# Performance work log

Measured on AMD Instinct MI355X. Metric: run time of the kernel, lower is better.

The kernel has to match this reference:

```python
import jax, jax.numpy as jnp
import numpy as np

N_PER_G, G = 2048, 2
N = N_PER_G * G
CIN, COUT, WIDTH, K = 128, 256, 64, 16
R_BASE, BOX, SLOPE = 1.8, 16.0, 0.1
R1, L1, O1 = 1.5 * R_BASE, 5, WIDTH // 2
R2, L2, O2 = R_BASE, 7, WIDTH // 4
R3, L3, O3 = 0.75 * R_BASE, 11, WIDTH // 4


def _build_edges(pos, batch, r):
    srcs, dsts = [], []
    for g in range(G):
        idx = np.nonzero(batch == g)[0]
        p = pos[idx]
        d2 = ((p[:, None, :] - p[None, :, :]) ** 2).sum(-1)
        i, j = np.nonzero(d2 <= r * r)  # includes self-pairs, like torch_cluster.radius
        dsts.append(idx[i]); srcs.append(idx[j])
    return (np.concatenate(srcs).astype(np.int32), np.concatenate(dsts).astype(np.int32))


def setup_inputs() -> dict:
    rng = np.random.default_rng(0)
    pos = (rng.random((N, 3)) * BOX).astype(np.float32)
    batch = np.repeat(np.arange(G), N_PER_G).astype(np.int32)
    seq = np.tile(np.arange(N_PER_G), G).astype(np.int32)
    ori = np.linalg.qr(rng.standard_normal((N, 3, 3)))[0].reshape(N, 9).astype(np.float32)
    x = rng.standard_normal((N, CIN)).astype(np.float32)
    s1, d1 = _build_edges(pos, batch, R1)
    s2, d2 = _build_edges(pos, batch, R2)
    s3, d3 = _build_edges(pos, batch, R3)
    def p(*shape):
        return jnp.asarray((rng.standard_normal(shape) * 0.05).astype(np.float32))
    return dict(
        x=jnp.asarray(x), pos=jnp.asarray(pos), ori=jnp.asarray(ori),
        seq=jnp.asarray(seq), batch=jnp.asarray(batch),
        src1=jnp.asarray(s1), dst1=jnp.asarray(d1),
        src2=jnp.asarray(s2), dst2=jnp.asarray(d2),
        src3=jnp.asarray(s3), dst3=jnp.asarray(d3),
        id_bn_g=jnp.ones(CIN), id_bn_b=jnp.zeros(CIN), id_W=p(CIN, COUT),
        in_bn_g=jnp.ones(CIN), in_bn_b=jnp.zeros(CIN), in_W=p(CIN, WIDTH),
        mid_bn_g=jnp.ones(WIDTH), mid_bn_b=jnp.zeros(WIDTH),
        Ws1=p(L1, 7, K), bs1=p(L1, K), W1=p(K * WIDTH, O1),
        Ws2=p(L2, 7, K), bs2=p(L2, K), W2=p(K * WIDTH, O2),
        Ws3=p(L3, 7, K), bs3=p(L3, K), W3=p(K * WIDTH, O3),
        out_bn_g=jnp.ones(WIDTH), out_bn_b=jnp.zeros(WIDTH), out_W=p(WIDTH, COUT),
    )


def _bn(x, g, b):
    # BatchNorm1d forward with batch statistics (biased variance), eps=1e-5
    m = jnp.mean(x, axis=0)
    v = jnp.mean((x - m) ** 2, axis=0)
    return (x - m) * jax.lax.rsqrt(v + 1e-5) * g + b


def _cdconv(h, pos, seq, ori, src, dst, r, l, Ws, bs, W):
    # src = sender j, dst = receiver i
    delta = pos[src] - pos[dst]                               # [E,3]
    dist = jnp.linalg.norm(delta, axis=-1, keepdims=True)     # [E,1]
    dirn = delta / (dist + 1e-9)
    fr_i = ori[dst].reshape(-1, 3, 3)
    fr_j = ori[src].reshape(-1, 3, 3)
    pos_feat = jnp.einsum('eij,ej->ei', fr_i, dirn)           # direction in receiver's local frame
    ori_feat = jnp.sum(fr_i * fr_j, axis=-1)                  # frame-axis dot products [E,3]
    feat = jnp.concatenate([dist / r, pos_feat, ori_feat], axis=-1)  # [E,7]
    hl = l // 2
    idx = jnp.clip(seq[src] - seq[dst], -hl, hl) + hl         # discrete sequential bin in [0,l-1]
    w = jax.nn.leaky_relu(jnp.einsum('ec,eck->ek', feat, Ws[idx]) + bs[idx], 0.2)  # [E,K]
    msg = (w[:, :, None] * h[src][:, None, :]).reshape(w.shape[0], -1)  # [E, K*C]
    agg = jax.ops.segment_sum(msg, dst, num_segments=h.shape[0])        # [N, K*C]
    return agg @ W


def _forward(x, pos, ori, seq, src1, dst1, src2, dst2, src3, dst3,
             id_bn_g, id_bn_b, id_W, in_bn_g, in_bn_b, in_W, mid_bn_g, mid_bn_b,
             Ws1, bs1, W1, Ws2, bs2, W2, Ws3, bs3, W3, out_bn_g, out_bn_b, out_W):
    identity = jax.nn.leaky_relu(_bn(x, id_bn_g, id_bn_b), SLOPE) @ id_W
    h = jax.nn.leaky_relu(_bn(x, in_bn_g, in_bn_b), SLOPE) @ in_W
    h = jax.nn.leaky_relu(_bn(h, mid_bn_g, mid_bn_b), SLOPE)
    x1 = _cdconv(h, pos, seq, ori, src1, dst1, R1, L1, Ws1, bs1, W1)
    x2 = _cdconv(h, pos, seq, ori, src2, dst2, R2, L2, Ws2, bs2, W2)
    x3 = _cdconv(h, pos, seq, ori, src3, dst3, R3, L3, Ws3, bs3, W3)
    cat = jnp.concatenate([x1, x2, x3], axis=1)               # [N, WIDTH]
    return jax.nn.leaky_relu(_bn(cat, out_bn_g, out_bn_b), SLOPE) @ out_W + identity


def reference(x, pos, ori, seq, batch, src1, dst1, src2, dst2, src3, dst3,
              id_bn_g, id_bn_b, id_W, in_bn_g, in_bn_b, in_W, mid_bn_g, mid_bn_b,
              Ws1, bs1, W1, Ws2, bs2, W2, Ws3, bs3, W3, out_bn_g, out_bn_b, out_W):
    return _forward(x, pos, ori, seq, src1, dst1, src2, dst2, src3, dst3,
                    id_bn_g, id_bn_b, id_W, in_bn_g, in_bn_b, in_W, mid_bn_g, mid_bn_b,
                    Ws1, bs1, W1, Ws2, bs2, W2, Ws3, bs3, W3, out_bn_g, out_bn_b, out_W)
```

## Files before the change

kernel.cpp:

```cpp
#include <hip/hip_runtime.h>

#define N_NODES 4096
#define CIN     128
#define COUT    256
#define WIDTH   64
#define KDIM    16
#define SLOPE   0.1f
#define WSLOPE  0.2f
#define BN_EPS  1e-5f

typedef float float4u __attribute__((ext_vector_type(4), aligned(4)));

__device__ __forceinline__ float lrelu(float x, float s) { return x > 0.f ? x : s * x; }

struct EdgeP {
  const int* src; const int* dst;
  const float* Ws; const float* bs;
  float* wbuf; int E; float inv_r; int hl;
};

#define WS_LD 113
#define BS_LD 17
#define NB_STATSX 32
#define NB_ROWPTR 49

__global__ __launch_bounds__(256) void prep_kernel(
    const float* __restrict__ x,
    const float* __restrict__ id_g, const float* __restrict__ id_b,
    const float* __restrict__ in_g, const float* __restrict__ in_b,
    float* __restrict__ sA, float* __restrict__ hA,
    float* __restrict__ sB, float* __restrict__ hB,
    int* __restrict__ rowp,
    EdgeP e0, EdgeP e1, EdgeP e2,
    const float* __restrict__ pos, const float* __restrict__ ori,
    const int* __restrict__ seq,
    int nb1, int nb2)
{
  int bx = blockIdx.x, t = threadIdx.x;

  if (bx < NB_STATSX) {
    int cg = bx;
    int lane = t & 63, wv = t >> 6;
    float s[4] = {0.f, 0.f, 0.f, 0.f}, q[4] = {0.f, 0.f, 0.f, 0.f};
    for (int r = t; r < N_NODES; r += 256) {
      float4u a = *(const float4u*)(x + (size_t)r * CIN + cg * 4);
      float v[4] = {a.x, a.y, a.z, a.w};
#pragma unroll
      for (int i = 0; i < 4; i++) { s[i] += v[i]; q[i] += v[i] * v[i]; }
    }
#pragma unroll
    for (int m = 1; m < 64; m <<= 1) {
#pragma unroll
      for (int i = 0; i < 4; i++) { s[i] += __shfl_xor(s[i], m, 64); q[i] += __shfl_xor(q[i], m, 64); }
    }
    __shared__ float rs[4][4], rq[4][4];
    if (lane == 0) {
#pragma unroll
      for (int i = 0; i < 4; i++) { rs[wv][i] = s[i]; rq[wv][i] = q[i]; }
    }
    __syncthreads();
    if (t < 4) {
      float S = rs[0][t] + rs[1][t] + rs[2][t] + rs[3][t];
      float Q = rq[0][t] + rq[1][t] + rq[2][t] + rq[3][t];
      float m = S / N_NODES;
      float v = Q / N_NODES - m * m;
      float rsv = rsqrtf(v + BN_EPS);
      int c = cg * 4 + t;
      float sa = id_g[c] * rsv;
      float sb = in_g[c] * rsv;
      sA[c] = sa; hA[c] = id_b[c] - m * sa;
      sB[c] = sb; hB[c] = in_b[c] - m * sb;
    }
    return;
  }

  if (bx < NB_STATSX + NB_ROWPTR) {
    int idx = (bx - NB_STATSX) * 256 + t;
    if (idx >= 3 * (N_NODES + 1)) return;
    int b = idx / (N_NODES + 1);
    int n = idx % (N_NODES + 1);
    const int* d = (b == 0) ? e0.dst : (b == 1) ? e1.dst : e2.dst;
    int E = (b == 0) ? e0.E : (b == 1) ? e1.E : e2.E;
    int lo = 0, hi = E;
    if (n >= N_NODES) lo = E;
    else {
      while (lo < hi) { int mid = (lo + hi) >> 1; if (d[mid] < n) lo = mid + 1; else hi = mid; }
    }
    rowp[(size_t)b * (N_NODES + 1) + n] = lo;
    return;
  }

  int eb = bx - (NB_STATSX + NB_ROWPTR);
  EdgeP p;
  int base;
  if (eb < nb1)            { p = e0; base = eb; }
  else if (eb < nb1 + nb2) { p = e1; base = eb - nb1; }
  else                     { p = e2; base = eb - nb1 - nb2; }

  __shared__ float wsl[11 * WS_LD];
  __shared__ float bsl[11 * BS_LD];
  int L = 2 * p.hl + 1;
  for (int i = t; i < L * 112; i += 256) {
    int bin = i / 112, r = i - bin * 112;
    wsl[bin * WS_LD + r] = p.Ws[(size_t)bin * 112 + r];
  }
  for (int i = t; i < L * 16; i += 256) {
    int bin = i >> 4, r = i & 15;
    bsl[bin * BS_LD + r] = p.bs[(size_t)bin * 16 + r];
  }
  __syncthreads();

  int e = base * 256 + t;
  if (e >= p.E) return;
  int j = p.src[e], i = p.dst[e];
  float px = pos[j * 3 + 0] - pos[i * 3 + 0];
  float py = pos[j * 3 + 1] - pos[i * 3 + 1];
  float pz = pos[j * 3 + 2] - pos[i * 3 + 2];
  float fi[9], fj[9];
  {
    float4u a0 = *(const float4u*)(ori + (size_t)i * 9);
    float4u a1 = *(const float4u*)(ori + (size_t)i * 9 + 4);
    fi[0] = a0.x; fi[1] = a0.y; fi[2] = a0.z; fi[3] = a0.w;
    fi[4] = a1.x; fi[5] = a1.y; fi[6] = a1.z; fi[7] = a1.w;
    fi[8] = ori[(size_t)i * 9 + 8];
    float4u b0 = *(const float4u*)(ori + (size_t)j * 9);
    float4u b1 = *(const float4u*)(ori + (size_t)j * 9 + 4);
    fj[0] = b0.x; fj[1] = b0.y; fj[2] = b0.z; fj[3] = b0.w;
    fj[4] = b1.x; fj[5] = b1.y; fj[6] = b1.z; fj[7] = b1.w;
    fj[8] = ori[(size_t)j * 9 + 8];
  }
  float dist = sqrtf(px * px + py * py + pz * pz);
  float inv = 1.0f / (dist + 1e-9f);
  float dx = px * inv, dy = py * inv, dz = pz * inv;
  float feat[7];
  feat[0] = dist * p.inv_r;
  feat[1] = fi[0] * dx + fi[1] * dy + fi[2] * dz;
  feat[2] = fi[3] * dx + fi[4] * dy + fi[5] * dz;
  feat[3] = fi[6] * dx + fi[7] * dy + fi[8] * dz;
  feat[4] = fi[0] * fj[0] + fi[1] * fj[1] + fi[2] * fj[2];
  feat[5] = fi[3] * fj[3] + fi[4] * fj[4] + fi[5] * fj[5];
  feat[6] = fi[6] * fj[6] + fi[7] * fj[7] + fi[8] * fj[8];
  int d = seq[j] - seq[i];
  d = d < -p.hl ? -p.hl : (d > p.hl ? p.hl : d);
  int bin = d + p.hl;
  const float* Wp = wsl + bin * WS_LD;
  const float* bp = bsl + bin * BS_LD;
  float w16[KDIM];
#pragma unroll
  for (int k = 0; k < KDIM; k++) {
    float a = bp[k];
#pragma unroll
    for (int c = 0; c < 7; c++) a += feat[c] * Wp[c * KDIM + k];
    w16[k] = lrelu(a, WSLOPE);
  }
  float4* wb = (float4*)(p.wbuf + (size_t)e * KDIM);
#pragma unroll
  for (int k = 0; k < 4; k++)
    wb[k] = make_float4(w16[4 * k], w16[4 * k + 1], w16[4 * k + 2], w16[4 * k + 3]);
}

__global__ __launch_bounds__(256) void gemm2_kernel(
    const float* __restrict__ x,
    const float* __restrict__ sA, const float* __restrict__ hA,
    const float* __restrict__ sB, const float* __restrict__ hB,
    const float* __restrict__ idW, const float* __restrict__ inW,
    float* __restrict__ ident, float* __restrict__ hpre)
{
  int bx = blockIdx.x, t = threadIdx.x;
  __shared__ float at[8 * CIN];
  bool coutp = bx < 512;
  int n0 = (coutp ? bx : bx - 512) * 8;
  {
    int r = t >> 5, c4 = (t & 31) * 4;
    const float* S = coutp ? sA : sB;
    const float* H = coutp ? hA : hB;
    float4u xv = *(const float4u*)(x + (size_t)(n0 + r) * CIN + c4);
    float4u sv = *(const float4u*)(S + c4);
    float4u hv = *(const float4u*)(H + c4);
    float4u o;
    o.x = lrelu(xv.x * sv.x + hv.x, SLOPE);
    o.y = lrelu(xv.y * sv.y + hv.y, SLOPE);
    o.z = lrelu(xv.z * sv.z + hv.z, SLOPE);
    o.w = lrelu(xv.w * sv.w + hv.w, SLOPE);
    *(float4u*)(at + r * CIN + c4) = o;
  }
  __syncthreads();
  if (coutp) {
    float acc[8] = {0.f, 0.f, 0.f, 0.f, 0.f, 0.f, 0.f, 0.f};
    for (int k = 0; k < CIN; k += 4) {
      float w0 = idW[(size_t)(k + 0) * COUT + t];
      float w1 = idW[(size_t)(k + 1) * COUT + t];
      float w2 = idW[(size_t)(k + 2) * COUT + t];
      float w3 = idW[(size_t)(k + 3) * COUT + t];
#pragma unroll
      for (int r8 = 0; r8 < 8; r8++) {
        float4u a = *(const float4u*)(at + r8 * CIN + k);
        acc[r8] += a.x * w0 + a.y * w1 + a.z * w2 + a.w * w3;
      }
    }
#pragma unroll
    for (int r8 = 0; r8 < 8; r8++) ident[(size_t)(n0 + r8) * COUT + t] = acc[r8];
  } else {
    int j = t & 63, g = t >> 6;
    float a0 = 0.f, a1 = 0.f;
    for (int k = 0; k < CIN; k += 4) {
      float w0 = inW[(size_t)(k + 0) * WIDTH + j];
      float w1 = inW[(size_t)(k + 1) * WIDTH + j];
      float w2 = inW[(size_t)(k + 2) * WIDTH + j];
      float w3 = inW[(size_t)(k + 3) * WIDTH + j];
      float4u u = *(const float4u*)(at + (2 * g) * CIN + k);
      float4u v = *(const float4u*)(at + (2 * g + 1) * CIN + k);
      a0 += u.x * w0 + u.y * w1 + u.z * w2 + u.w * w3;
      a1 += v.x * w0 + v.y * w1 + v.z * w2 + v.w * w3;
    }
    hpre[(size_t)(n0 + 2 * g) * WIDTH + j] = a0;
    hpre[(size_t)(n0 + 2 * g + 1) * WIDTH + j] = a1;
  }
}

__global__ __launch_bounds__(256) void stats_affine_kernel(
    const float* __restrict__ X, int C,
    const float* __restrict__ g, const float* __restrict__ b,
    float* __restrict__ s_out, float* __restrict__ h_out)
{
  int cg = blockIdx.x;
  int t = threadIdx.x, lane = t & 63, wv = t >> 6;
  float s[4] = {0.f, 0.f, 0.f, 0.f}, q[4] = {0.f, 0.f, 0.f, 0.f};
  for (int r = t; r < N_NODES; r += 256) {
    float4u a = *(const float4u*)(X + (size_t)r * C + cg * 4);
    float v[4] = {a.x, a.y, a.z, a.w};
#pragma unroll
    for (int i = 0; i < 4; i++) { s[i] += v[i]; q[i] += v[i] * v[i]; }
  }
#pragma unroll
  for (int m = 1; m < 64; m <<= 1) {
#pragma unroll
    for (int i = 0; i < 4; i++) { s[i] += __shfl_xor(s[i], m, 64); q[i] += __shfl_xor(q[i], m, 64); }
  }
  __shared__ float rs[4][4], rq[4][4];
  if (lane == 0) {
#pragma unroll
    for (int i = 0; i < 4; i++) { rs[wv][i] = s[i]; rq[wv][i] = q[i]; }
  }
  __syncthreads();
  if (t < 4) {
    float S = rs[0][t] + rs[1][t] + rs[2][t] + rs[3][t];
    float Q = rq[0][t] + rq[1][t] + rq[2][t] + rq[3][t];
    float m = S / N_NODES;
    float v = Q / N_NODES - m * m;
    int c = cg * 4 + t;
    float sv = g[c] * rsqrtf(v + BN_EPS);
    s_out[c] = sv;
    h_out[c] = b[c] - m * sv;
  }
}

struct AggP {
  const int* src; const float* wbuf; const float* Wf;
  int O; int coloff;
};

#define ALD 68

__global__ __launch_bounds__(256) void agg3_kernel(
    AggP p0, AggP p1, AggP p2, const int* __restrict__ rowp,
    const float* __restrict__ hpre,
    const float* __restrict__ sH, const float* __restrict__ hH,
    float* __restrict__ cat)
{
  int b = blockIdx.y;
  AggP p = (b == 0) ? p0 : (b == 1) ? p1 : p2;
  int n = blockIdx.x, t = threadIdx.x, lane = t & 63, wv = t >> 6;

  __shared__ float lds[4][KDIM * ALD];
  __shared__ float pw[4][WIDTH];

  float scH = sH[lane], shH = hH[lane];
  const int* rp = rowp + (size_t)b * (N_NODES + 1);
  int start = rp[n], end = rp[n + 1];

  float acc[KDIM];
#pragma unroll
  for (int k = 0; k < KDIM; k++) acc[k] = 0.f;

  int e = start + wv;
  for (; e + 12 < end; e += 16) {
    int j0 = __builtin_amdgcn_readfirstlane(p.src[e]);
    int j1 = __builtin_amdgcn_readfirstlane(p.src[e + 4]);
    int j2 = __builtin_amdgcn_readfirstlane(p.src[e + 8]);
    int j3 = __builtin_amdgcn_readfirstlane(p.src[e + 12]);
    float r0 = hpre[(size_t)j0 * WIDTH + lane];
    float r1 = hpre[(size_t)j1 * WIDTH + lane];
    float r2 = hpre[(size_t)j2 * WIDTH + lane];
    float r3 = hpre[(size_t)j3 * WIDTH + lane];
    const float4* a0 = (const float4*)(p.wbuf + (size_t)e * KDIM);
    const float4* a1 = (const float4*)(p.wbuf + (size_t)(e + 4) * KDIM);
    const float4* a2 = (const float4*)(p.wbuf + (size_t)(e + 8) * KDIM);
    const float4* a3 = (const float4*)(p.wbuf + (size_t)(e + 12) * KDIM);
    float4 w00 = a0[0], w01 = a0[1], w02 = a0[2], w03 = a0[3];
    float4 w10 = a1[0], w11 = a1[1], w12 = a1[2], w13 = a1[3];
    float4 w20 = a2[0], w21 = a2[1], w22 = a2[2], w23 = a2[3];
    float4 w30 = a3[0], w31 = a3[1], w32 = a3[2], w33 = a3[3];
    float hj0 = lrelu(r0 * scH + shH, SLOPE);
    float hj1 = lrelu(r1 * scH + shH, SLOPE);
    float hj2 = lrelu(r2 * scH + shH, SLOPE);
    float hj3 = lrelu(r3 * scH + shH, SLOPE);
    acc[0] += w00.x * hj0; acc[1] += w00.y * hj0; acc[2] += w00.z * hj0; acc[3] += w00.w * hj0;
    acc[4] += w01.x * hj0; acc[5] += w01.y * hj0; acc[6] += w01.z * hj0; acc[7] += w01.w * hj0;
    acc[8] += w02.x * hj0; acc[9] += w02.y * hj0; acc[10] += w02.z * hj0; acc[11] += w02.w * hj0;
    acc[12] += w03.x * hj0; acc[13] += w03.y * hj0; acc[14] += w03.z * hj0; acc[15] += w03.w * hj0;
    acc[0] += w10.x * hj1; acc[1] += w10.y * hj1; acc[2] += w10.z * hj1; acc[3] += w10.w * hj1;
    acc[4] += w11.x * hj1; acc[5] += w11.y * hj1; acc[6] += w11.z * hj1; acc[7] += w11.w * hj1;
    acc[8] += w12.x * hj1; acc[9] += w12.y * hj1; acc[10] += w12.z * hj1; acc[11] += w12.w * hj1;
    acc[12] += w13.x * hj1; acc[13] += w13.y * hj1; acc[14] += w13.z * hj1; acc[15] += w13.w * hj1;
    acc[0] += w20.x * hj2; acc[1] += w20.y * hj2; acc[2] += w20.z * hj2; acc[3] += w20.w * hj2;
    acc[4] += w21.x * hj2; acc[5] += w21.y * hj2; acc[6] += w21.z * hj2; acc[7] += w21.w * hj2;
    acc[8] += w22.x * hj2; acc[9] += w22.y * hj2; acc[10] += w22.z * hj2; acc[11] += w22.w * hj2;
    acc[12] += w23.x * hj2; acc[13] += w23.y * hj2; acc[14] += w23.z * hj2; acc[15] += w23.w * hj2;
    acc[0] += w30.x * hj3; acc[1] += w30.y * hj3; acc[2] += w30.z * hj3; acc[3] += w30.w * hj3;
    acc[4] += w31.x * hj3; acc[5] += w31.y * hj3; acc[6] += w31.z * hj3; acc[7] += w31.w * hj3;
    acc[8] += w32.x * hj3; acc[9] += w32.y * hj3; acc[10] += w32.z * hj3; acc[11] += w32.w * hj3;
    acc[12] += w33.x * hj3; acc[13] += w33.y * hj3; acc[14] += w33.z * hj3; acc[15] += w33.w * hj3;
  }
  for (; e < end; e += 4) {
    int j = __builtin_amdgcn_readfirstlane(p.src[e]);
    float hr = hpre[(size_t)j * WIDTH + lane];
    const float4* w4 = (const float4*)(p.wbuf + (size_t)e * KDIM);
    float4 w0 = w4[0], w1 = w4[1], w2 = w4[2], w3 = w4[3];
    float hj = lrelu(hr * scH + shH, SLOPE);
    acc[0] += w0.x * hj; acc[1] += w0.y * hj; acc[2] += w0.z * hj; acc[3] += w0.w * hj;
    acc[4] += w1.x * hj; acc[5] += w1.y * hj; acc[6] += w1.z * hj; acc[7] += w1.w * hj;
    acc[8] += w2.x * hj; acc[9] += w2.y * hj; acc[10] += w2.z * hj; acc[11] += w2.w * hj;
    acc[12] += w3.x * hj; acc[13] += w3.y * hj; acc[14] += w3.z * hj; acc[15] += w3.w * hj;
  }

#pragma unroll
  for (int k = 0; k < KDIM; k++) lds[wv][k * ALD + lane] = acc[k];
  __syncthreads();

  for (int i = t; i < KDIM * ALD; i += 256)
    lds[0][i] = lds[0][i] + lds[1][i] + lds[2][i] + lds[3][i];
  __syncthreads();

  int O = p.O;
  int o = t & (O - 1);
  int q = t / O;
  int kpg = O >> 4;
  float part = 0.f;
  for (int kk = 0; kk < kpg; kk++) {
    int k = q * kpg + kk;
    const float* ar = lds[0] + k * ALD;
    const float* wf = p.Wf + (size_t)(k * WIDTH) * O + o;
    for (int c = 0; c < WIDTH; c += 4) {
      float4 a = *(const float4*)(ar + c);
      part += a.x * wf[(size_t)(c + 0) * O];
      part += a.y * wf[(size_t)(c + 1) * O];
      part += a.z * wf[(size_t)(c + 2) * O];
      part += a.w * wf[(size_t)(c + 3) * O];
    }
  }
  for (int m = O; m < 64; m <<= 1) part += __shfl_xor(part, m, 64);
  if (lane < O) pw[wv][lane] = part;
  __syncthreads();
  if (t < O)
    cat[(size_t)n * WIDTH + p.coloff + t] = pw[0][t] + pw[1][t] + pw[2][t] + pw[3][t];
}

__global__ __launch_bounds__(256) void final_kernel(
    const float* __restrict__ cat,
    const float* __restrict__ sC, const float* __restrict__ hC,
    const float* __restrict__ outW,
    const float* __restrict__ identity, float* __restrict__ out)
{
  int t = threadIdx.x;
  int n0 = blockIdx.x * 8;
  __shared__ float cn8[8 * WIDTH];
#pragma unroll
  for (int s = 0; s < 2; s++) {
    int ii = s * 256 + t;
    int r = ii >> 6, k = ii & 63;
    cn8[ii] = lrelu(cat[(size_t)(n0 + r) * WIDTH + k] * sC[k] + hC[k], SLOPE);
  }
  __syncthreads();
  float acc[8];
#pragma unroll
  for (int r = 0; r < 8; r++) acc[r] = identity[(size_t)(n0 + r) * COUT + t];
  for (int k = 0; k < WIDTH; k += 4) {
    float w0 = outW[(size_t)(k + 0) * COUT + t];
    float w1 = outW[(size_t)(k + 1) * COUT + t];
    float w2 = outW[(size_t)(k + 2) * COUT + t];
    float w3 = outW[(size_t)(k + 3) * COUT + t];
#pragma unroll
    for (int r = 0; r < 8; r++) {
      float4u a = *(const float4u*)(cn8 + r * WIDTH + k);
      acc[r] += a.x * w0 + a.y * w1 + a.z * w2 + a.w * w3;
    }
  }
#pragma unroll
  for (int r = 0; r < 8; r++) out[(size_t)(n0 + r) * COUT + t] = acc[r];
}

extern "C" void kernel_launch(void* const* d_in, const int* in_sizes, int n_in,
                              void* d_out, int out_size, void* d_ws, size_t ws_size,
                              hipStream_t stream) {
  const float* x    = (const float*)d_in[0];
  const float* pos  = (const float*)d_in[1];
  const float* ori  = (const float*)d_in[2];
  const int* seq  = (const int*)d_in[3];
  const int* src1 = (const int*)d_in[5];  const int* dst1 = (const int*)d_in[6];
  const int* src2 = (const int*)d_in[7];  const int* dst2 = (const int*)d_in[8];
  const int* src3 = (const int*)d_in[9];  const int* dst3 = (const int*)d_in[10];
  const float* id_g  = (const float*)d_in[11]; const float* id_b  = (const float*)d_in[12];
  const float* id_W  = (const float*)d_in[13];
  const float* in_g  = (const float*)d_in[14]; const float* in_b  = (const float*)d_in[15];
  const float* in_W  = (const float*)d_in[16];
  const float* mid_g = (const float*)d_in[17]; const float* mid_b = (const float*)d_in[18];
  const float* Ws1   = (const float*)d_in[19]; const float* bs1   = (const float*)d_in[20];
  const float* W1    = (const float*)d_in[21];
  const float* Ws2   = (const float*)d_in[22]; const float* bs2   = (const float*)d_in[23];
  const float* W2    = (const float*)d_in[24];
  const float* Ws3   = (const float*)d_in[25]; const float* bs3   = (const float*)d_in[26];
  const float* W3    = (const float*)d_in[27];
  const float* out_g = (const float*)d_in[28]; const float* out_b = (const float*)d_in[29];
  const float* out_W = (const float*)d_in[30];

  const int E1 = in_sizes[5], E2 = in_sizes[7], E3 = in_sizes[9];

  float* wsp = (float*)d_ws;
  size_t off = 0;
  auto alloc = [&](size_t n) { float* p = wsp + off; off += (n + 63) & ~(size_t)63; return p; };
  float* sA   = alloc(CIN);   float* hA = alloc(CIN);
  float* sB   = alloc(CIN);   float* hB = alloc(CIN);
  float* sH   = alloc(WIDTH); float* hH = alloc(WIDTH);
  float* sC   = alloc(WIDTH); float* hC = alloc(WIDTH);
  float* ident = alloc((size_t)N_NODES * COUT);
  float* hpre  = alloc((size_t)N_NODES * WIDTH);
  float* catb  = alloc((size_t)N_NODES * WIDTH);
  int*   rowp  = (int*)alloc(3 * (N_NODES + 1));
  float* w1    = alloc((size_t)E1 * KDIM);
  float* w2    = alloc((size_t)E2 * KDIM);
  float* w3    = alloc((size_t)E3 * KDIM);
  (void)ws_size; (void)n_in; (void)out_size;

  int nb1 = (E1 + 255) / 256, nb2 = (E2 + 255) / 256, nb3 = (E3 + 255) / 256;

  EdgeP e0{src1, dst1, Ws1, bs1, w1, E1, 1.0f / 2.70f, 2};
  EdgeP e1{src2, dst2, Ws2, bs2, w2, E2, 1.0f / 1.80f, 3};
  EdgeP e2{src3, dst3, Ws3, bs3, w3, E3, 1.0f / 1.35f, 5};

  prep_kernel<<<NB_STATSX + NB_ROWPTR + nb1 + nb2 + nb3, 256, 0, stream>>>(
      x, id_g, id_b, in_g, in_b, sA, hA, sB, hB, rowp,
      e0, e1, e2, pos, ori, seq, nb1, nb2);
  gemm2_kernel<<<1024, 256, 0, stream>>>(x, sA, hA, sB, hB, id_W, in_W, ident, hpre);
  stats_affine_kernel<<<WIDTH / 4, 256, 0, stream>>>(hpre, WIDTH, mid_g, mid_b, sH, hH);
  AggP a0{src1, w1, W1, 32, 0};
  AggP a1{src2, w2, W2, 16, 32};
  AggP a2{src3, w3, W3, 16, 48};
  agg3_kernel<<<dim3(N_NODES, 3), 256, 0, stream>>>(a0, a1, a2, rowp, hpre, sH, hH, catb);
  stats_affine_kernel<<<WIDTH / 4, 256, 0, stream>>>(catb, WIDTH, out_g, out_b, sC, hC);
  final_kernel<<<N_NODES / 8, 256, 0, stream>>>(catb, sC, hC, out_W, ident, (float*)d_out);
}
```

Measured before the change: 233.9 us.

## Fuse BN stats into producers via atomics; aggregate four nodes per block

Removes both stats_affine kernel launches. Their column sums and sums of squares are now accumulated with atomicAdd at the end of gemm2 and agg3, and the scale and shift are recomputed locally in the consumer kernels. agg3 now gives each wave its own node (4 nodes per block) instead of splitting one node's edges across four waves, so the cross-wave LDS reduction goes away and each Wf load is reused for four nodes. The cost is atomic contention on 256 floats, non-deterministic summation order, and possible imbalance when nodes have very different degrees.

```diff
diff --git a/kernel.cpp b/kernel.cpp
--- a/kernel.cpp
+++ b/kernel.cpp
@@ -13,6 +13,7 @@
 
 __device__ __forceinline__ float lrelu(float x, float s) { return x > 0.f ? x : s * x; }
 
+
 struct EdgeP {
   const int* src; const int* dst;
   const float* Ws; const float* bs;
@@ -30,7 +31,7 @@
     const float* __restrict__ in_g, const float* __restrict__ in_b,
     float* __restrict__ sA, float* __restrict__ hA,
     float* __restrict__ sB, float* __restrict__ hB,
-    int* __restrict__ rowp,
+    int* __restrict__ rowp, float* __restrict__ accum,
     EdgeP e0, EdgeP e1, EdgeP e2,
     const float* __restrict__ pos, const float* __restrict__ ori,
     const int* __restrict__ seq,
@@ -39,6 +40,7 @@
   int bx = blockIdx.x, t = threadIdx.x;
 
   if (bx < NB_STATSX) {
+    if (bx == 0) accum[t] = 0.f;
     int cg = bx;
     int lane = t & 63, wv = t >> 6;
     float s[4] = {0.f, 0.f, 0.f, 0.f}, q[4] = {0.f, 0.f, 0.f, 0.f};
@@ -164,7 +166,8 @@
     const float* __restrict__ sA, const float* __restrict__ hA,
     const float* __restrict__ sB, const float* __restrict__ hB,
     const float* __restrict__ idW, const float* __restrict__ inW,
-    float* __restrict__ ident, float* __restrict__ hpre)
+    float* __restrict__ ident, float* __restrict__ hpre,
+    float* __restrict__ accum)
 {
   int bx = blockIdx.x, t = threadIdx.x;
   __shared__ float at[8 * CIN];
@@ -215,43 +218,14 @@
     }
     hpre[(size_t)(n0 + 2 * g) * WIDTH + j] = a0;
     hpre[(size_t)(n0 + 2 * g + 1) * WIDTH + j] = a1;
-  }
-}
-
-__global__ __launch_bounds__(256) void stats_affine_kernel(
-    const float* __restrict__ X, int C,
-    const float* __restrict__ g, const float* __restrict__ b,
-    float* __restrict__ s_out, float* __restrict__ h_out)
-{
-  int cg = blockIdx.x;
-  int t = threadIdx.x, lane = t & 63, wv = t >> 6;
-  float s[4] = {0.f, 0.f, 0.f, 0.f}, q[4] = {0.f, 0.f, 0.f, 0.f};
-  for (int r = t; r < N_NODES; r += 256) {
-    float4u a = *(const float4u*)(X + (size_t)r * C + cg * 4);
-    float v[4] = {a.x, a.y, a.z, a.w};
-#pragma unroll
-    for (int i = 0; i < 4; i++) { s[i] += v[i]; q[i] += v[i] * v[i]; }
-  }
-#pragma unroll
-  for (int m = 1; m < 64; m <<= 1) {
-#pragma unroll
-    for (int i = 0; i < 4; i++) { s[i] += __shfl_xor(s[i], m, 64); q[i] += __shfl_xor(q[i], m, 64); }
-  }
-  __shared__ float rs[4][4], rq[4][4];
-  if (lane == 0) {
-#pragma unroll
-    for (int i = 0; i < 4; i++) { rs[wv][i] = s[i]; rq[wv][i] = q[i]; }
-  }
-  __syncthreads();
-  if (t < 4) {
-    float S = rs[0][t] + rs[1][t] + rs[2][t] + rs[3][t];
-    float Q = rq[0][t] + rq[1][t] + rq[2][t] + rq[3][t];
-    float m = S / N_NODES;
-    float v = Q / N_NODES - m * m;
-    int c = cg * 4 + t;
-    float sv = g[c] * rsqrtf(v + BN_EPS);
-    s_out[c] = sv;
-    h_out[c] = b[c] - m * sv;
+    __shared__ float ps[4][WIDTH], pq[4][WIDTH];
+    ps[g][j] = a0 + a1;
+    pq[g][j] = a0 * a0 + a1 * a1;
+    __syncthreads();
+    if (t < WIDTH) {
+      atomicAdd(&accum[t],      ps[0][t] + ps[1][t] + ps[2][t] + ps[3][t]);
+      atomicAdd(&accum[64 + t], pq[0][t] + pq[1][t] + pq[2][t] + pq[3][t]);
+    }
   }
 }
 
@@ -261,46 +235,53 @@
 };
 
 #define ALD 68
+#define STRIP (KDIM * ALD + 4)
 
 __global__ __launch_bounds__(256) void agg3_kernel(
     AggP p0, AggP p1, AggP p2, const int* __restrict__ rowp,
     const float* __restrict__ hpre,
-    const float* __restrict__ sH, const float* __restrict__ hH,
-    float* __restrict__ cat)
+    const float* __restrict__ mid_g, const float* __restrict__ mid_b,
+    float* __restrict__ accum, float* __restrict__ cat)
 {
   int b = blockIdx.y;
   AggP p = (b == 0) ? p0 : (b == 1) ? p1 : p2;
-  int n = blockIdx.x, t = threadIdx.x, lane = t & 63, wv = t >> 6;
-
-  __shared__ float lds[4][KDIM * ALD];
-  __shared__ float pw[4][WIDTH];
-
-  float scH = sH[lane], shH = hH[lane];
+  int n0 = blockIdx.x * 4, t = threadIdx.x, lane = t & 63, wv = t >> 6;
+
+  __shared__ float lds[4 * STRIP];
+  __shared__ float pw[4][4][32];
+  __shared__ float sHl[WIDTH], hHl[WIDTH];
+  if (t < WIDTH) {
+    float m = accum[t] * (1.f / N_NODES);
+    float v = accum[64 + t] * (1.f / N_NODES) - m * m;
+    float s = mid_g[t] * rsqrtf(v + BN_EPS);
+    sHl[t] = s; hHl[t] = mid_b[t] - m * s;
+  }
+  __syncthreads();
+  float scH = sHl[lane], shH = hHl[lane];
+
   const int* rp = rowp + (size_t)b * (N_NODES + 1);
+  int n = n0 + wv;
   int start = rp[n], end = rp[n + 1];
 
   float acc[KDIM];
 #pragma unroll
   for (int k = 0; k < KDIM; k++) acc[k] = 0.f;
 
-  int e = start + wv;
-  for (; e + 12 < end; e += 16) {
+  int e = start;
+  for (; e + 3 < end; e += 4) {
     int j0 = __builtin_amdgcn_readfirstlane(p.src[e]);
-    int j1 = __builtin_amdgcn_readfirstlane(p.src[e + 4]);
-    int j2 = __builtin_amdgcn_readfirstlane(p.src[e + 8]);
-    int j3 = __builtin_amdgcn_readfirstlane(p.src[e + 12]);
+    int j1 = __builtin_amdgcn_readfirstlane(p.src[e + 1]);
+    int j2 = __builtin_amdgcn_readfirstlane(p.src[e + 2]);
+    int j3 = __builtin_amdgcn_readfirstlane(p.src[e + 3]);
     float r0 = hpre[(size_t)j0 * WIDTH + lane];
     float r1 = hpre[(size_t)j1 * WIDTH + lane];
     float r2 = hpre[(size_t)j2 * WIDTH + lane];
     float r3 = hpre[(size_t)j3 * WIDTH + lane];
     const float4* a0 = (const float4*)(p.wbuf + (size_t)e * KDIM);
-    const float4* a1 = (const float4*)(p.wbuf + (size_t)(e + 4) * KDIM);
-    const float4* a2 = (const float4*)(p.wbuf + (size_t)(e + 8) * KDIM);
-    const float4* a3 = (const float4*)(p.wbuf + (size_t)(e + 12) * KDIM);
-    float4 w00 = a0[0], w01 = a0[1], w02 = a0[2], w03 = a0[3];
-    float4 w10 = a1[0], w11 = a1[1], w12 = a1[2], w13 = a1[3];
-    float4 w20 = a2[0], w21 = a2[1], w22 = a2[2], w23 = a2[3];
-    float4 w30 = a3[0], w31 = a3[1], w32 = a3[2], w33 = a3[3];
+    float4 w00 = a0[0], w01 = a0[1], w02 = a0[2],  w03 = a0[3];
+    float4 w10 = a0[4], w11 = a0[5], w12 = a0[6],  w13 = a0[7];
+    float4 w20 = a0[8], w21 = a0[9], w22 = a0[10], w23 = a0[11];
+    float4 w30 = a0[12], w31 = a0[13], w32 = a0[14], w33 = a0[15];
     float hj0 = lrelu(r0 * scH + shH, SLOPE);
     float hj1 = lrelu(r1 * scH + shH, SLOPE);
     float hj2 = lrelu(r2 * scH + shH, SLOPE);
@@ -322,7 +303,7 @@
     acc[8] += w32.x * hj3; acc[9] += w32.y * hj3; acc[10] += w32.z * hj3; acc[11] += w32.w * hj3;
     acc[12] += w33.x * hj3; acc[13] += w33.y * hj3; acc[14] += w33.z * hj3; acc[15] += w33.w * hj3;
   }
-  for (; e < end; e += 4) {
+  for (; e < end; e++) {
     int j = __builtin_amdgcn_readfirstlane(p.src[e]);
     float hr = hpre[(size_t)j * WIDTH + lane];
     const float4* w4 = (const float4*)(p.wbuf + (size_t)e * KDIM);
@@ -335,46 +316,65 @@
   }
 
 #pragma unroll
-  for (int k = 0; k < KDIM; k++) lds[wv][k * ALD + lane] = acc[k];
-  __syncthreads();
-
-  for (int i = t; i < KDIM * ALD; i += 256)
-    lds[0][i] = lds[0][i] + lds[1][i] + lds[2][i] + lds[3][i];
+  for (int k = 0; k < KDIM; k++) lds[wv * STRIP + k * ALD + lane] = acc[k];
   __syncthreads();
 
   int O = p.O;
   int o = t & (O - 1);
   int q = t / O;
   int kpg = O >> 4;
-  float part = 0.f;
+  float part[4] = {0.f, 0.f, 0.f, 0.f};
   for (int kk = 0; kk < kpg; kk++) {
     int k = q * kpg + kk;
-    const float* ar = lds[0] + k * ALD;
     const float* wf = p.Wf + (size_t)(k * WIDTH) * O + o;
     for (int c = 0; c < WIDTH; c += 4) {
-      float4 a = *(const float4*)(ar + c);
-      part += a.x * wf[(size_t)(c + 0) * O];
-      part += a.y * wf[(size_t)(c + 1) * O];
-      part += a.z * wf[(size_t)(c + 2) * O];
-      part += a.w * wf[(size_t)(c + 3) * O];
-    }
-  }
-  for (int m = O; m < 64; m <<= 1) part += __shfl_xor(part, m, 64);
-  if (lane < O) pw[wv][lane] = part;
-  __syncthreads();
-  if (t < O)
-    cat[(size_t)n * WIDTH + p.coloff + t] = pw[0][t] + pw[1][t] + pw[2][t] + pw[3][t];
+      float w0 = wf[(size_t)(c + 0) * O];
+      float w1 = wf[(size_t)(c + 1) * O];
+      float w2 = wf[(size_t)(c + 2) * O];
+      float w3 = wf[(size_t)(c + 3) * O];
+#pragma unroll
+      for (int r = 0; r < 4; r++) {
+        float4 a = *(const float4*)(lds + r * STRIP + k * ALD + c);
+        part[r] += a.x * w0 + a.y * w1 + a.z * w2 + a.w * w3;
+      }
+    }
+  }
+  for (int m = O; m < 64; m <<= 1) {
+#pragma unroll
+    for (int r = 0; r < 4; r++) part[r] += __shfl_xor(part[r], m, 64);
+  }
+  if (lane < O) {
+#pragma unroll
+    for (int r = 0; r < 4; r++) pw[wv][r][lane] = part[r];
+  }
+  __syncthreads();
+  if (t < 4 * O) {
+    int r = t / O, o2 = t % O;
+    float v = pw[0][r][o2] + pw[1][r][o2] + pw[2][r][o2] + pw[3][r][o2];
+    cat[(size_t)(n0 + r) * WIDTH + p.coloff + o2] = v;
+    atomicAdd(&accum[128 + p.coloff + o2], v);
+    atomicAdd(&accum[192 + p.coloff + o2], v * v);
+  }
 }
 
 __global__ __launch_bounds__(256) void final_kernel(
     const float* __restrict__ cat,
-    const float* __restrict__ sC, const float* __restrict__ hC,
+    const float* __restrict__ out_g, const float* __restrict__ out_b,
+    const float* __restrict__ accum,
     const float* __restrict__ outW,
     const float* __restrict__ identity, float* __restrict__ out)
 {
   int t = threadIdx.x;
   int n0 = blockIdx.x * 8;
+  __shared__ float sC[WIDTH], hC[WIDTH];
   __shared__ float cn8[8 * WIDTH];
+  if (t < WIDTH) {
+    float m = accum[128 + t] * (1.f / N_NODES);
+    float v = accum[192 + t] * (1.f / N_NODES) - m * m;
+    float s = out_g[t] * rsqrtf(v + BN_EPS);
+    sC[t] = s; hC[t] = out_b[t] - m * s;
+  }
+  __syncthreads();
 #pragma unroll
   for (int s = 0; s < 2; s++) {
     int ii = s * 256 + t;
@@ -429,10 +429,9 @@
   float* wsp = (float*)d_ws;
   size_t off = 0;
   auto alloc = [&](size_t n) { float* p = wsp + off; off += (n + 63) & ~(size_t)63; return p; };
+  float* accum = alloc(256);
   float* sA   = alloc(CIN);   float* hA = alloc(CIN);
   float* sB   = alloc(CIN);   float* hB = alloc(CIN);
-  float* sH   = alloc(WIDTH); float* hH = alloc(WIDTH);
-  float* sC   = alloc(WIDTH); float* hC = alloc(WIDTH);
   float* ident = alloc((size_t)N_NODES * COUT);
   float* hpre  = alloc((size_t)N_NODES * WIDTH);
   float* catb  = alloc((size_t)N_NODES * WIDTH);
@@ -449,14 +448,14 @@
   EdgeP e2{src3, dst3, Ws3, bs3, w3, E3, 1.0f / 1.35f, 5};
 
   prep_kernel<<<NB_STATSX + NB_ROWPTR + nb1 + nb2 + nb3, 256, 0, stream>>>(
-      x, id_g, id_b, in_g, in_b, sA, hA, sB, hB, rowp,
+      x, id_g, id_b, in_g, in_b, sA, hA, sB, hB, rowp, accum,
       e0, e1, e2, pos, ori, seq, nb1, nb2);
-  gemm2_kernel<<<1024, 256, 0, stream>>>(x, sA, hA, sB, hB, id_W, in_W, ident, hpre);
-  stats_affine_kernel<<<WIDTH / 4, 256, 0, stream>>>(hpre, WIDTH, mid_g, mid_b, sH, hH);
+  gemm2_kernel<<<1024, 256, 0, stream>>>(x, sA, hA, sB, hB, id_W, in_W, ident, hpre, accum);
   AggP a0{src1, w1, W1, 32, 0};
   AggP a1{src2, w2, W2, 16, 32};
   AggP a2{src3, w3, W3, 16, 48};
-  agg3_kernel<<<dim3(N_NODES, 3), 256, 0, stream>>>(a0, a1, a2, rowp, hpre, sH, hH, catb);
-  stats_affine_kernel<<<WIDTH / 4, 256, 0, stream>>>(catb, WIDTH, out_g, out_b, sC, hC);
-  final_kernel<<<N_NODES / 8, 256, 0, stream>>>(catb, sC, hC, out_W, ident, (float*)d_out);
+  agg3_kernel<<<dim3(N_NODES / 4, 3), 256, 0, stream>>>(a0, a1, a2, rowp, hpre,
+                                                        mid_g, mid_b, accum, catb);
+  final_kernel<<<N_NODES / 8, 256, 0, stream>>>(catb, out_g, out_b, accum, out_W,
+                                                ident, (float*)d_out);
 }
```

Measured after the change: 529.7 us. 126% more time.

## Fuse BatchNorm statistics into producer kernels via striped atomic accumulators

Applied to the files above, without the earlier changes.

Removes the two standalone stats_affine kernels by accumulating per-channel sum and sum-of-squares with atomics into 32 striped buffers inside gemm2 (for hpre) and agg3 (for cat). The buffers are zeroed in prep_kernel. Consumers (agg3, final) reduce the stripes and compute the scale/shift themselves, which saves two launches and two full re-reads of the activations. In exchange it adds atomic traffic and a redundant per-block reduction over 32 stripes in every agg3 and final block, and the float atomics make summation order nondeterministic.

```diff
diff --git a/kernel.cpp b/kernel.cpp
--- a/kernel.cpp
+++ b/kernel.cpp
@@ -8,6 +8,7 @@
 #define SLOPE   0.1f
 #define WSLOPE  0.2f
 #define BN_EPS  1e-5f
+#define NSTRIPE 32
 
 typedef float float4u __attribute__((ext_vector_type(4), aligned(4)));
 
@@ -30,7 +31,7 @@
     const float* __restrict__ in_g, const float* __restrict__ in_b,
     float* __restrict__ sA, float* __restrict__ hA,
     float* __restrict__ sB, float* __restrict__ hB,
-    int* __restrict__ rowp,
+    int* __restrict__ rowp, float* __restrict__ accum,
     EdgeP e0, EdgeP e1, EdgeP e2,
     const float* __restrict__ pos, const float* __restrict__ ori,
     const int* __restrict__ seq,
@@ -39,6 +40,7 @@
   int bx = blockIdx.x, t = threadIdx.x;
 
   if (bx < NB_STATSX) {
+    accum[bx * 256 + t] = 0.f;
     int cg = bx;
     int lane = t & 63, wv = t >> 6;
     float s[4] = {0.f, 0.f, 0.f, 0.f}, q[4] = {0.f, 0.f, 0.f, 0.f};
@@ -164,7 +166,8 @@
     const float* __restrict__ sA, const float* __restrict__ hA,
     const float* __restrict__ sB, const float* __restrict__ hB,
     const float* __restrict__ idW, const float* __restrict__ inW,
-    float* __restrict__ ident, float* __restrict__ hpre)
+    float* __restrict__ ident, float* __restrict__ hpre,
+    float* __restrict__ accum)
 {
   int bx = blockIdx.x, t = threadIdx.x;
   __shared__ float at[8 * CIN];
@@ -215,43 +218,15 @@
     }
     hpre[(size_t)(n0 + 2 * g) * WIDTH + j] = a0;
     hpre[(size_t)(n0 + 2 * g + 1) * WIDTH + j] = a1;
-  }
-}
-
-__global__ __launch_bounds__(256) void stats_affine_kernel(
-    const float* __restrict__ X, int C,
-    const float* __restrict__ g, const float* __restrict__ b,
-    float* __restrict__ s_out, float* __restrict__ h_out)
-{
-  int cg = blockIdx.x;
-  int t = threadIdx.x, lane = t & 63, wv = t >> 6;
-  float s[4] = {0.f, 0.f, 0.f, 0.f}, q[4] = {0.f, 0.f, 0.f, 0.f};
-  for (int r = t; r < N_NODES; r += 256) {
-    float4u a = *(const float4u*)(X + (size_t)r * C + cg * 4);
-    float v[4] = {a.x, a.y, a.z, a.w};
-#pragma unroll
-    for (int i = 0; i < 4; i++) { s[i] += v[i]; q[i] += v[i] * v[i]; }
-  }
-#pragma unroll
-  for (int m = 1; m < 64; m <<= 1) {
-#pragma unroll
-    for (int i = 0; i < 4; i++) { s[i] += __shfl_xor(s[i], m, 64); q[i] += __shfl_xor(q[i], m, 64); }
-  }
-  __shared__ float rs[4][4], rq[4][4];
-  if (lane == 0) {
-#pragma unroll
-    for (int i = 0; i < 4; i++) { rs[wv][i] = s[i]; rq[wv][i] = q[i]; }
-  }
-  __syncthreads();
-  if (t < 4) {
-    float S = rs[0][t] + rs[1][t] + rs[2][t] + rs[3][t];
-    float Q = rq[0][t] + rq[1][t] + rq[2][t] + rq[3][t];
-    float m = S / N_NODES;
-    float v = Q / N_NODES - m * m;
-    int c = cg * 4 + t;
-    float sv = g[c] * rsqrtf(v + BN_EPS);
-    s_out[c] = sv;
-    h_out[c] = b[c] - m * sv;
+    __shared__ float ps[4][WIDTH], pq[4][WIDTH];
+    ps[g][j] = a0 + a1;
+    pq[g][j] = a0 * a0 + a1 * a1;
+    __syncthreads();
+    if (t < WIDTH) {
+      float* as = accum + (bx & (NSTRIPE - 1)) * 256;
+      atomicAdd(&as[t],      ps[0][t] + ps[1][t] + ps[2][t] + ps[3][t]);
+      atomicAdd(&as[64 + t], pq[0][t] + pq[1][t] + pq[2][t] + pq[3][t]);
+    }
   }
 }
 
@@ -265,8 +240,8 @@
 __global__ __launch_bounds__(256) void agg3_kernel(
     AggP p0, AggP p1, AggP p2, const int* __restrict__ rowp,
     const float* __restrict__ hpre,
-    const float* __restrict__ sH, const float* __restrict__ hH,
-    float* __restrict__ cat)
+    const float* __restrict__ mid_g, const float* __restrict__ mid_b,
+    float* __restrict__ accum, float* __restrict__ cat)
 {
   int b = blockIdx.y;
   AggP p = (b == 0) ? p0 : (b == 1) ? p1 : p2;
@@ -274,8 +249,22 @@
 
   __shared__ float lds[4][KDIM * ALD];
   __shared__ float pw[4][WIDTH];
-
-  float scH = sH[lane], shH = hH[lane];
+  __shared__ float sHl[WIDTH], hHl[WIDTH];
+  if (t < WIDTH) {
+    float S = 0.f, Q = 0.f;
+#pragma unroll
+    for (int s = 0; s < NSTRIPE; s++) {
+      S += accum[s * 256 + t];
+      Q += accum[s * 256 + 64 + t];
+    }
+    float m = S * (1.f / N_NODES);
+    float v = Q * (1.f / N_NODES) - m * m;
+    float sc = mid_g[t] * rsqrtf(v + BN_EPS);
+    sHl[t] = sc; hHl[t] = mid_b[t] - m * sc;
+  }
+  __syncthreads();
+  float scH = sHl[lane], shH = hHl[lane];
+
   const int* rp = rowp + (size_t)b * (N_NODES + 1);
   int start = rp[n], end = rp[n + 1];
 
@@ -362,19 +351,39 @@
   for (int m = O; m < 64; m <<= 1) part += __shfl_xor(part, m, 64);
   if (lane < O) pw[wv][lane] = part;
   __syncthreads();
-  if (t < O)
-    cat[(size_t)n * WIDTH + p.coloff + t] = pw[0][t] + pw[1][t] + pw[2][t] + pw[3][t];
+  if (t < O) {
+    float v = pw[0][t] + pw[1][t] + pw[2][t] + pw[3][t];
+    cat[(size_t)n * WIDTH + p.coloff + t] = v;
+    float* as = accum + (n & (NSTRIPE - 1)) * 256;
+    atomicAdd(&as[128 + p.coloff + t], v);
+    atomicAdd(&as[192 + p.coloff + t], v * v);
+  }
 }
 
 __global__ __launch_bounds__(256) void final_kernel(
     const float* __restrict__ cat,
-    const float* __restrict__ sC, const float* __restrict__ hC,
+    const float* __restrict__ out_g, const float* __restrict__ out_b,
+    const float* __restrict__ accum,
     const float* __restrict__ outW,
     const float* __restrict__ identity, float* __restrict__ out)
 {
   int t = threadIdx.x;
   int n0 = blockIdx.x * 8;
+  __shared__ float sC[WIDTH], hC[WIDTH];
   __shared__ float cn8[8 * WIDTH];
+  if (t < WIDTH) {
+    float S = 0.f, Q = 0.f;
+#pragma unroll
+    for (int s = 0; s < NSTRIPE; s++) {
+      S += accum[s * 256 + 128 + t];
+      Q += accum[s * 256 + 192 + t];
+    }
+    float m = S * (1.f / N_NODES);
+    float v = Q * (1.f / N_NODES) - m * m;
+    float sc = out_g[t] * rsqrtf(v + BN_EPS);
+    sC[t] = sc; hC[t] = out_b[t] - m * sc;
+  }
+  __syncthreads();
 #pragma unroll
   for (int s = 0; s < 2; s++) {
     int ii = s * 256 + t;
@@ -429,10 +438,9 @@
   float* wsp = (float*)d_ws;
   size_t off = 0;
   auto alloc = [&](size_t n) { float* p = wsp + off; off += (n + 63) & ~(size_t)63; return p; };
+  float* accum = alloc(NSTRIPE * 256);
   float* sA   = alloc(CIN);   float* hA = alloc(CIN);
   float* sB   = alloc(CIN);   float* hB = alloc(CIN);
-  float* sH   = alloc(WIDTH); float* hH = alloc(WIDTH);
-  float* sC   = alloc(WIDTH); float* hC = alloc(WIDTH);
   float* ident = alloc((size_t)N_NODES * COUT);
   float* hpre  = alloc((size_t)N_NODES * WIDTH);
   float* catb  = alloc((size_t)N_NODES * WIDTH);
@@ -449,14 +457,14 @@
   EdgeP e2{src3, dst3, Ws3, bs3, w3, E3, 1.0f / 1.35f, 5};
 
   prep_kernel<<<NB_STATSX + NB_ROWPTR + nb1 + nb2 + nb3, 256, 0, stream>>>(
-      x, id_g, id_b, in_g, in_b, sA, hA, sB, hB, rowp,
+      x, id_g, id_b, in_g, in_b, sA, hA, sB, hB, rowp, accum,
       e0, e1, e2, pos, ori, seq, nb1, nb2);
-  gemm2_kernel<<<1024, 256, 0, stream>>>(x, sA, hA, sB, hB, id_W, in_W, ident, hpre);
-  stats_affine_kernel<<<WIDTH / 4, 256, 0, stream>>>(hpre, WIDTH, mid_g, mid_b, sH, hH);
+  gemm2_kernel<<<1024, 256, 0, stream>>>(x, sA, hA, sB, hB, id_W, in_W, ident, hpre, accum);
   AggP a0{src1, w1, W1, 32, 0};
   AggP a1{src2, w2, W2, 16, 32};
   AggP a2{src3, w3, W3, 16, 48};
-  agg3_kernel<<<dim3(N_NODES, 3), 256, 0, stream>>>(a0, a1, a2, rowp, hpre, sH, hH, catb);
-  stats_affine_kernel<<<WIDTH / 4, 256, 0, stream>>>(catb, WIDTH, out_g, out_b, sC, hC);
-  final_kernel<<<N_NODES / 8, 256, 0, stream>>>(catb, sC, hC, out_W, ident, (float*)d_out);
+  agg3_kernel<<<dim3(N_NODES, 3), 256, 0, stream>>>(a0, a1, a2, rowp, hpre,
+                                                    mid_g, mid_b, accum, catb);
+  final_kernel<<<N_NODES / 8, 256, 0, stream>>>(catb, out_g, out_b, accum, out_W,
+                                                ident, (float*)d_out);
 }
```

Measured after the change: 233.0 us. About the same (-0.4%).

## Process two nodes per block in agg3 to reuse projection weights

Applied to the files above, without the earlier changes.

The aggregation kernel now handles two destination nodes per block, with two waves per node splitting that node's edges. In the final projection each weight value loaded from global memory is applied to both nodes' aggregated features, halving weight traffic per node and halving the block count. In exchange, each node's edge loop has only two waves instead of four, so per-node latency hiding drops and nodes with different degrees can leave waves unbalanced.

```diff
diff --git a/kernel.cpp b/kernel.cpp
--- a/kernel.cpp
+++ b/kernel.cpp
@@ -270,12 +270,17 @@
 {
   int b = blockIdx.y;
   AggP p = (b == 0) ? p0 : (b == 1) ? p1 : p2;
-  int n = blockIdx.x, t = threadIdx.x, lane = t & 63, wv = t >> 6;
+  int nA = blockIdx.x * 2, t = threadIdx.x, lane = t & 63, wv = t >> 6;
 
   __shared__ float lds[4][KDIM * ALD];
-  __shared__ float pw[4][WIDTH];
-
-  float scH = sH[lane], shH = hH[lane];
+  __shared__ float pw[4][2][32];
+  __shared__ float sHl[WIDTH], hHl[WIDTH];
+  if (t < WIDTH) { sHl[t] = sH[t]; hHl[t] = hH[t]; }
+  __syncthreads();
+  float scH = sHl[lane], shH = hHl[lane];
+
+  int n = nA + (wv >> 1);
+  int sub = wv & 1;
   const int* rp = rowp + (size_t)b * (N_NODES + 1);
   int start = rp[n], end = rp[n + 1];
 
@@ -283,20 +288,20 @@
 #pragma unroll
   for (int k = 0; k < KDIM; k++) acc[k] = 0.f;
 
-  int e = start + wv;
-  for (; e + 12 < end; e += 16) {
+  int e = start + sub;
+  for (; e + 6 < end; e += 8) {
     int j0 = __builtin_amdgcn_readfirstlane(p.src[e]);
-    int j1 = __builtin_amdgcn_readfirstlane(p.src[e + 4]);
-    int j2 = __builtin_amdgcn_readfirstlane(p.src[e + 8]);
-    int j3 = __builtin_amdgcn_readfirstlane(p.src[e + 12]);
+    int j1 = __builtin_amdgcn_readfirstlane(p.src[e + 2]);
+    int j2 = __builtin_amdgcn_readfirstlane(p.src[e + 4]);
+    int j3 = __builtin_amdgcn_readfirstlane(p.src[e + 6]);
     float r0 = hpre[(size_t)j0 * WIDTH + lane];
     float r1 = hpre[(size_t)j1 * WIDTH + lane];
     float r2 = hpre[(size_t)j2 * WIDTH + lane];
     float r3 = hpre[(size_t)j3 * WIDTH + lane];
     const float4* a0 = (const float4*)(p.wbuf + (size_t)e * KDIM);
-    const float4* a1 = (const float4*)(p.wbuf + (size_t)(e + 4) * KDIM);
-    const float4* a2 = (const float4*)(p.wbuf + (size_t)(e + 8) * KDIM);
-    const float4* a3 = (const float4*)(p.wbuf + (size_t)(e + 12) * KDIM);
+    const float4* a1 = (const float4*)(p.wbuf + (size_t)(e + 2) * KDIM);
+    const float4* a2 = (const float4*)(p.wbuf + (size_t)(e + 4) * KDIM);
+    const float4* a3 = (const float4*)(p.wbuf + (size_t)(e + 6) * KDIM);
     float4 w00 = a0[0], w01 = a0[1], w02 = a0[2], w03 = a0[3];
     float4 w10 = a1[0], w11 = a1[1], w12 = a1[2], w13 = a1[3];
     float4 w20 = a2[0], w21 = a2[1], w22 = a2[2], w23 = a2[3];
@@ -322,7 +327,7 @@
     acc[8] += w32.x * hj3; acc[9] += w32.y * hj3; acc[10] += w32.z * hj3; acc[11] += w32.w * hj3;
     acc[12] += w33.x * hj3; acc[13] += w33.y * hj3; acc[14] += w33.z * hj3; acc[15] += w33.w * hj3;
   }
-  for (; e < end; e += 4) {
+  for (; e < end; e += 2) {
     int j = __builtin_amdgcn_readfirstlane(p.src[e]);
     float hr = hpre[(size_t)j * WIDTH + lane];
     const float4* w4 = (const float4*)(p.wbuf + (size_t)e * KDIM);
@@ -338,32 +343,44 @@
   for (int k = 0; k < KDIM; k++) lds[wv][k * ALD + lane] = acc[k];
   __syncthreads();
 
-  for (int i = t; i < KDIM * ALD; i += 256)
-    lds[0][i] = lds[0][i] + lds[1][i] + lds[2][i] + lds[3][i];
+  for (int i = t; i < KDIM * ALD; i += 256) {
+    lds[0][i] += lds[1][i];
+    lds[2][i] += lds[3][i];
+  }
   __syncthreads();
 
   int O = p.O;
   int o = t & (O - 1);
   int q = t / O;
   int kpg = O >> 4;
-  float part = 0.f;
+  float pA = 0.f, pB = 0.f;
   for (int kk = 0; kk < kpg; kk++) {
     int k = q * kpg + kk;
-    const float* ar = lds[0] + k * ALD;
+    const float* arA = lds[0] + k * ALD;
+    const float* arB = lds[2] + k * ALD;
     const float* wf = p.Wf + (size_t)(k * WIDTH) * O + o;
     for (int c = 0; c < WIDTH; c += 4) {
-      float4 a = *(const float4*)(ar + c);
-      part += a.x * wf[(size_t)(c + 0) * O];
-      part += a.y * wf[(size_t)(c + 1) * O];
-      part += a.z * wf[(size_t)(c + 2) * O];
-      part += a.w * wf[(size_t)(c + 3) * O];
-    }
-  }
-  for (int m = O; m < 64; m <<= 1) part += __shfl_xor(part, m, 64);
-  if (lane < O) pw[wv][lane] = part;
-  __syncthreads();
-  if (t < O)
-    cat[(size_t)n * WIDTH + p.coloff + t] = pw[0][t] + pw[1][t] + pw[2][t] + pw[3][t];
+      float w0 = wf[(size_t)(c + 0) * O];
+      float w1 = wf[(size_t)(c + 1) * O];
+      float w2 = wf[(size_t)(c + 2) * O];
+      float w3 = wf[(size_t)(c + 3) * O];
+      float4 a = *(const float4*)(arA + c);
+      float4 bb = *(const float4*)(arB + c);
+      pA += a.x * w0 + a.y * w1 + a.z * w2 + a.w * w3;
+      pB += bb.x * w0 + bb.y * w1 + bb.z * w2 + bb.w * w3;
+    }
+  }
+  for (int m = O; m < 64; m <<= 1) {
+    pA += __shfl_xor(pA, m, 64);
+    pB += __shfl_xor(pB, m, 64);
+  }
+  if (lane < O) { pw[wv][0][lane] = pA; pw[wv][1][lane] = pB; }
+  __syncthreads();
+  if (t < 2 * O) {
+    int r = t / O, o2 = t % O;
+    cat[(size_t)(nA + r) * WIDTH + p.coloff + o2] =
+        pw[0][r][o2] + pw[1][r][o2] + pw[2][r][o2] + pw[3][r][o2];
+  }
 }
 
 __global__ __launch_bounds__(256) void final_kernel(
@@ -456,7 +473,7 @@
   AggP a0{src1, w1, W1, 32, 0};
   AggP a1{src2, w2, W2, 16, 32};
   AggP a2{src3, w3, W3, 16, 48};
-  agg3_kernel<<<dim3(N_NODES, 3), 256, 0, stream>>>(a0, a1, a2, rowp, hpre, sH, hH, catb);
+  agg3_kernel<<<dim3(N_NODES / 2, 3), 256, 0, stream>>>(a0, a1, a2, rowp, hpre, sH, hH, catb);
   stats_affine_kernel<<<WIDTH / 4, 256, 0, stream>>>(catb, WIDTH, out_g, out_b, sC, hC);
   final_kernel<<<N_NODES / 8, 256, 0, stream>>>(catb, sC, hC, out_W, ident, (float*)d_out);
 }
```

Result: faster. 221.4 us (-5.3%).
